# Optimization experiments

Hardware: AMD Instinct MI355X
Metric: run time of the kernel (lower is better)

## Reference

```python
import jax, jax.numpy as jnp
import numpy as np

N, T, K, V, E = 64, 256, 64, 32000, 100


def setup_inputs() -> dict:
    key = jax.random.key(0)
    ks = jax.random.split(key, 7)
    x = jax.random.randint(ks[0], (N, T), 0, V)
    emb_weight = jax.random.normal(ks[1], (V, E), dtype=jnp.float32)
    # trans: Linear(E, K*K, bias=False), weight uniform(-1,1)
    W_trans = jax.random.uniform(ks[2], (K * K, E), minval=-1.0, maxval=1.0, dtype=jnp.float32)
    # start: Linear(1, K)
    start_w = jax.random.normal(ks[3], (K, 1), dtype=jnp.float32) * 0.1
    start_b = jax.random.normal(ks[4], (K,), dtype=jnp.float32) * 0.1
    # emb_cluster: Embedding(K, K)
    emb_cluster_w = jax.random.normal(ks[5], (K, K), dtype=jnp.float32)
    # vocab: Linear(K, V, bias=False), weight uniform(-1,1)
    vocab_w = jax.random.uniform(ks[6], (V, K), minval=-1.0, maxval=1.0, dtype=jnp.float32)
    return {"x": x, "emb_weight": emb_weight, "W_trans": W_trans,
            "start_w": start_w, "start_b": start_b,
            "emb_cluster_w": emb_cluster_w, "vocab_w": vocab_w}


def reference(x, emb_weight, W_trans, start_w, start_b, emb_cluster_w, vocab_w):
    n, t = x.shape
    k = emb_cluster_w.shape[0]
    # word embeddings used to condition transitions at steps 0..T-2
    xe = emb_weight[x[:, :-1]]                                   # [N,T-1,E]
    # transition log-probs: log_softmax over destination state
    tran = jax.nn.log_softmax(
        jnp.einsum('nte,ce->ntc', xe, W_trans).reshape(n, t - 1, k, k), axis=-1)
    # emission log-probs per cluster: E[k, v]
    Elog = jax.nn.log_softmax(emb_cluster_w @ vocab_w.T, axis=-1)  # [K,V]
    emit = Elog.T[x[:, 1:]]                                       # [N,T-1,K]
    # initial alpha: log_softmax(start(ones)) expanded over batch
    alpha0 = jax.nn.log_softmax(start_w[:, 0] + start_b)           # [K]
    alpha0 = jnp.broadcast_to(alpha0[None, :], (n, k))
    tran_t = jnp.moveaxis(tran, 1, 0)   # [T-1,N,K,K]
    emit_t = jnp.moveaxis(emit, 1, 0)   # [T-1,N,K]

    def step(alpha, te):
        tr, em = te
        # logsumexp over previous state j: alpha[n,j] + tr[n,j,k]
        a = jax.scipy.special.logsumexp(alpha[:, :, None] + tr, axis=1) + em
        return a, None

    alpha, _ = jax.lax.scan(step, alpha0, (tran_t, emit_t))
    return -jnp.mean(jax.scipy.special.logsumexp(alpha, axis=1))
```

## Files before the change

kernel.cpp:

```cpp
#include <hip/hip_runtime.h>
#include <hip/hip_bf16.h>
#include <stdint.h>

#define NT 16320
#define NTPAD 16384
#define KDIM 128
#define NCOLS 4096
#define NSEQ 64
#define TSTEPS 255
#define VOCAB 32000
#define EDIM 100
#define CHUNKS 17
#define CLEN 15

typedef __attribute__((ext_vector_type(8))) short s8v;
typedef __attribute__((ext_vector_type(4))) float f4v;

__device__ __forceinline__ float bflo(uint32_t u) { return __uint_as_float(u << 16); }
__device__ __forceinline__ float bfhi(uint32_t u) { return __uint_as_float(u & 0xffff0000u); }

__device__ __forceinline__ void load_lds16(const void* g, void* l) {
    __builtin_amdgcn_global_load_lds(
        (const __attribute__((address_space(1))) void*)(uintptr_t)g,
        (__attribute__((address_space(3))) void*)(uintptr_t)l,
        16, 0, 0);
}

__global__ __launch_bounds__(256) void prep_dk(const int* __restrict__ x,
                                               const float* __restrict__ emb,
                                               const float* __restrict__ Wt,
                                               const float* __restrict__ ec,
                                               const float* __restrict__ vw,
                                               __hip_bfloat16* __restrict__ A,
                                               __hip_bfloat16* __restrict__ B,
                                               float* __restrict__ partials) {
    int bid = blockIdx.x;
    int tid = threadIdx.x;
    if (bid < 1280) {
        int rloc = tid >> 4, q = tid & 15;
        int b = bid * 16 + rloc;
        int c0 = q * 8;
        float vals[8] = {0.f, 0.f, 0.f, 0.f, 0.f, 0.f, 0.f, 0.f};
        __hip_bfloat16* dst;
        if (b < NTPAD) {
            if (b < NT) {
                int n = b / TSTEPS;
                int t = b - n * TSTEPS;
                int tok = x[n * 256 + t];
                const float* er = emb + (size_t)tok * EDIM;
#pragma unroll
                for (int i = 0; i < 8; ++i) { int e = c0 + i; if (e < EDIM) vals[i] = er[e]; }
            }
            dst = A + (size_t)b * KDIM + c0;
        } else {
            int cc = b - NTPAD;
            const float* wr = Wt + (size_t)cc * EDIM;
#pragma unroll
            for (int i = 0; i < 8; ++i) { int e = c0 + i; if (e < EDIM) vals[i] = wr[e]; }
            dst = B + (size_t)cc * KDIM + c0;
        }
        union { __hip_bfloat16 h[8]; uint4 u; } pk;
#pragma unroll
        for (int i = 0; i < 8; ++i) pk.h[i] = __float2bfloat16(vals[i]);
        *(uint4*)dst = pk.u;
    } else {
        int db = bid - 1280;
        int wave = tid >> 6, lane = tid & 63;
        float er[64];
        {
            const float4* ecv = (const float4*)(ec + (size_t)lane * 64);
#pragma unroll
            for (int i = 0; i < 16; ++i) {
                float4 v = ecv[i];
                er[4 * i] = v.x; er[4 * i + 1] = v.y; er[4 * i + 2] = v.z; er[4 * i + 3] = v.w;
            }
        }
        int v0 = db * 125;
        float m = -1e30f, s = 0.f;
        for (int v = v0 + wave; v < v0 + 125; v += 4) {
            int vu = __builtin_amdgcn_readfirstlane(v);
            const float* row = vw + (size_t)vu * 64;
            float acc = 0.f;
#pragma unroll
            for (int e = 0; e < 64; ++e) acc += er[e] * row[e];
            float nm = fmaxf(m, acc);
            s = s * __expf(m - nm) + __expf(acc - nm);
            m = nm;
        }
        __shared__ float pm[4][64], ps[4][64];
        pm[wave][lane] = m; ps[wave][lane] = s;
        __syncthreads();
        if (tid < 64) {
            float M = pm[0][tid], Ssum = ps[0][tid];
#pragma unroll
            for (int w = 1; w < 4; ++w) {
                float m2 = pm[w][tid], s2 = ps[w][tid];
                float nm = fmaxf(M, m2);
                Ssum = Ssum * __expf(M - nm) + s2 * __expf(m2 - nm);
                M = nm;
            }
            partials[(db * 64 + tid) * 2]     = M;
            partials[(db * 64 + tid) * 2 + 1] = Ssum;
        }
    }
}

__global__ __launch_bounds__(256) void emit_kern(const int* __restrict__ x,
                                                 const float* __restrict__ ec,
                                                 const float* __restrict__ vw,
                                                 const float* __restrict__ partials,
                                                 __hip_bfloat16* __restrict__ emB) {
    __shared__ float pm[4][64], ps[4][64], sD[64];
    int tid = threadIdx.x;
    int wave = tid >> 6, lane = tid & 63;

    {
        float M = -1e30f, S = 0.f;
        for (int b = wave; b < 256; b += 4) {
            float m2 = partials[(b * 64 + lane) * 2];
            float s2 = partials[(b * 64 + lane) * 2 + 1];
            float nm = fmaxf(M, m2);
            S = S * __expf(M - nm) + s2 * __expf(m2 - nm);
            M = nm;
        }
        pm[wave][lane] = M; ps[wave][lane] = S;
    }

    float er[64];
    {
        const float4* ecv = (const float4*)(ec + (size_t)lane * 64);
#pragma unroll
        for (int i = 0; i < 16; ++i) {
            float4 v = ecv[i];
            er[4 * i] = v.x; er[4 * i + 1] = v.y; er[4 * i + 2] = v.z; er[4 * i + 3] = v.w;
        }
    }
    __syncthreads();
    if (tid < 64) {
        float M = pm[0][tid], S = ps[0][tid];
#pragma unroll
        for (int w = 1; w < 4; ++w) {
            float m2 = pm[w][tid], s2 = ps[w][tid];
            float nm = fmaxf(M, m2);
            S = S * __expf(M - nm) + s2 * __expf(m2 - nm);
            M = nm;
        }
        sD[tid] = M + __logf(S);
    }
    __syncthreads();

    float dj = sD[lane];
    int j = lane;
    int pos = ((j >> 2) & 3) * 16 + ((j >> 4) & 3) * 4 + (j & 3);
    int nt0 = blockIdx.x * 32 + wave * 8;
#pragma unroll
    for (int s = 0; s < 8; ++s) {
        int nt = nt0 + s;
        int n = nt / TSTEPS;
        int t = nt - n * TSTEPS;
        int tok = x[n * 256 + t + 1];
        tok = __builtin_amdgcn_readfirstlane(tok);
        const float* row = vw + (size_t)tok * 64;
        float acc = 0.f;
#pragma unroll
        for (int e = 0; e < 64; ++e) acc += er[e] * row[e];
        emB[(size_t)nt * 64 + pos] = __float2bfloat16(__expf(acc - dj));
    }
}

__global__ __launch_bounds__(256) void gemm_kern(const __hip_bfloat16* __restrict__ A,
                                                 const __hip_bfloat16* __restrict__ B,
                                                 const __hip_bfloat16* __restrict__ emB,
                                                 __hip_bfloat16* __restrict__ Eg) {
    int mblk = blockIdx.x;
    int nblk = blockIdx.y;
    int tid = threadIdx.x, wave = tid >> 6, lane = tid & 63;

    __shared__ __align__(16) char smem[65536];
    char* sA = smem;
    char* sB = smem + 32768;

    {
        int r0 = wave * 32;
        int l16 = lane & 15;
        int rsub = lane >> 4;
#pragma unroll
        for (int g = 0; g < 8; ++g) {
            int r = r0 + g * 4 + rsub;
            int chunk = l16 ^ (r & 7);
            const char* gp = (const char*)(A + (size_t)(mblk * 128 + r) * KDIM) + chunk * 16;
            load_lds16(gp, sA + (r0 + g * 4) * 256);
        }
#pragma unroll
        for (int g = 0; g < 8; ++g) {
            int c = r0 + g * 4 + rsub;
            int chunk = l16 ^ (c & 7);
            const char* gp = (const char*)(B + (size_t)(nblk * 128 + c) * KDIM) + chunk * 16;
            load_lds16(gp, sB + (r0 + g * 4) * 256);
        }
    }
    __syncthreads();

    int wc = (wave >> 1) * 64, wm = (wave & 1) * 64;
    int l15 = lane & 15, g4 = lane >> 4;
    f4v acc[4][4] = {};
#pragma unroll
    for (int k32 = 0; k32 < 4; ++k32) {
        s8v af[4], bf[4];
#pragma unroll
        for (int jt = 0; jt < 4; ++jt) {
            int r = wc + jt * 16 + l15;
            int chunk = (k32 * 4 + g4) ^ (r & 7);
            af[jt] = *(const s8v*)(sB + r * 256 + chunk * 16);
        }
#pragma unroll
        for (int mt = 0; mt < 4; ++mt) {
            int r = wm + mt * 16 + l15;
            int chunk = (k32 * 4 + g4) ^ (r & 7);
            bf[mt] = *(const s8v*)(sA + r * 256 + chunk * 16);
        }
#pragma unroll
        for (int jt = 0; jt < 4; ++jt)
#pragma unroll
            for (int mt = 0; mt < 4; ++mt)
                acc[jt][mt] = __builtin_amdgcn_mfma_f32_16x16x32_bf16(af[jt], bf[mt], acc[jt][mt], 0, 0, 0);
    }
    __syncthreads();

    char* sW = smem;
    const char* emb8 = (const char*)emB;
#pragma unroll
    for (int mt = 0; mt < 4; ++mt) {
        int mrow = wm + mt * 16 + l15;
        int mglob = mblk * 128 + mrow;
        float v[16];
#pragma unroll
        for (int jt = 0; jt < 4; ++jt)
#pragma unroll
            for (int rr = 0; rr < 4; ++rr) v[jt * 4 + rr] = acc[jt][mt][rr];
        float mx = v[0];
#pragma unroll
        for (int k = 1; k < 16; ++k) mx = fmaxf(mx, v[k]);
        mx = fmaxf(mx, __shfl_xor(mx, 16, 64));
        mx = fmaxf(mx, __shfl_xor(mx, 32, 64));
        float ex[16], sg = 0.f;
#pragma unroll
        for (int k = 0; k < 16; ++k) { ex[k] = __expf(v[k] - mx); sg += ex[k]; }
        sg += __shfl_xor(sg, 16, 64);
        sg += __shfl_xor(sg, 32, 64);
        float inv = 1.0f / sg;
        uint4 e0 = *(const uint4*)(emb8 + (size_t)mglob * 128 + g4 * 32);
        uint4 e1 = *(const uint4*)(emb8 + (size_t)mglob * 128 + g4 * 32 + 16);
        float em[16];
        {
            const uint32_t* w0 = (const uint32_t*)&e0;
            const uint32_t* w1 = (const uint32_t*)&e1;
#pragma unroll
            for (int i = 0; i < 4; ++i) {
                em[2 * i] = bflo(w0[i]);     em[2 * i + 1] = bfhi(w0[i]);
                em[8 + 2 * i] = bflo(w1[i]); em[8 + 2 * i + 1] = bfhi(w1[i]);
            }
        }
#pragma unroll
        for (int jt = 0; jt < 4; ++jt) {
            union { __hip_bfloat16 h[4]; uint2 u; } pk;
#pragma unroll
            for (int rr = 0; rr < 4; ++rr)
                pk.h[rr] = __float2bfloat16(ex[jt * 4 + rr] * inv * em[jt * 4 + rr]);
            *(uint2*)(sW + mrow * 272 + (wc + jt * 16 + g4 * 4) * 2) = pk.u;
        }
    }
    __syncthreads();

    {
        int rloc = tid >> 3;
        int q = tid & 7;
#pragma unroll
        for (int rp = 0; rp < 4; ++rp) {
            int row = rp * 32 + rloc;
            char* dst = (char*)Eg + (size_t)(mblk * 128 + row) * 8192 + nblk * 256;
            const char* src = sW + row * 272;
            *(uint4*)(dst + q * 16)       = *(const uint4*)(src + q * 16);
            *(uint4*)(dst + 128 + q * 16) = *(const uint4*)(src + 128 + q * 16);
        }
    }
}

__global__ __launch_bounds__(64) void chunk_kern(const __hip_bfloat16* __restrict__ Eg,
                                                 __hip_bfloat16* __restrict__ Gout,
                                                 float* __restrict__ Rout,
                                                 float* __restrict__ out) {
    int lane = threadIdx.x;
    if (blockIdx.x == 0 && lane == 0) *out = 0.f;
    int l15 = lane & 15, g4 = lane >> 4;
    int id = blockIdx.x;
    int n = (id * 3856) >> 16;
    int c = id - n * 17;
    int base_m = n * TSTEPS + c * CLEN;

    __shared__ __align__(16) char sGT[64 * 144];

    {
        uint4 z = {0, 0, 0, 0};
#pragma unroll
        for (int i = 0; i < 8; ++i) *(uint4*)(sGT + lane * 144 + i * 16) = z;
        *(uint16_t*)(sGT + lane * 144 + lane * 2) = 0x3F80;
    }

    const char* Ebase = (const char*)Eg;
    uint4 pf[4][2];
    {
        const char* tp = Ebase + (size_t)(base_m + 14) * 8192;
#pragma unroll
        for (int at = 0; at < 4; ++at)
#pragma unroll
            for (int kk = 0; kk < 2; ++kk)
                pf[at][kk] = *(const uint4*)(tp + (at * 16 + l15) * 128 + kk * 64 + g4 * 16);
    }

    float rlog[4] = {0.f, 0.f, 0.f, 0.f};

    for (int tl = 14; tl >= 0; --tl) {
        uint4 af[4][2];
#pragma unroll
        for (int at = 0; at < 4; ++at) { af[at][0] = pf[at][0]; af[at][1] = pf[at][1]; }
        if (tl > 0) {
            const char* tp = Ebase + (size_t)(base_m + tl - 1) * 8192;
#pragma unroll
            for (int at = 0; at < 4; ++at)
#pragma unroll
                for (int kk = 0; kk < 2; ++kk)
                    pf[at][kk] = *(const uint4*)(tp + (at * 16 + l15) * 128 + kk * 64 + g4 * 16);
        }

        f4v acc[4][4] = {};
#pragma unroll
        for (int kk = 0; kk < 2; ++kk) {
#pragma unroll
            for (int ct = 0; ct < 4; ++ct) {
                s8v b = *(const s8v*)(sGT + (ct * 16 + l15) * 144 + kk * 64 + g4 * 16);
#pragma unroll
                for (int at = 0; at < 4; ++at)
                    acc[at][ct] = __builtin_amdgcn_mfma_f32_16x16x32_bf16(
                        *(const s8v*)&af[at][kk], b, acc[at][ct], 0, 0, 0);
            }
        }

        if (tl % 3 == 0) {
#pragma unroll
            for (int ct = 0; ct < 4; ++ct) {
                float mx = acc[0][ct][0];
#pragma unroll
                for (int at = 0; at < 4; ++at)
#pragma unroll
                    for (int rr = 0; rr < 4; ++rr) mx = fmaxf(mx, acc[at][ct][rr]);
                mx = fmaxf(mx, __shfl_xor(mx, 16, 64));
                mx = fmaxf(mx, __shfl_xor(mx, 32, 64));
                mx = fmaxf(mx, 1e-38f);
                rlog[ct] += __logf(mx);
                float inv = 1.0f / mx;
                int col = ct * 16 + l15;
#pragma unroll
                for (int at = 0; at < 4; ++at) {
                    union { __hip_bfloat16 h[4]; uint2 u; } pk;
#pragma unroll
                    for (int rr = 0; rr < 4; ++rr)
                        pk.h[rr] = __float2bfloat16(acc[at][ct][rr] * inv);
                    *(uint2*)(sGT + col * 144 + at * 32 + g4 * 8) = pk.u;
                }
            }
        } else {
#pragma unroll
            for (int ct = 0; ct < 4; ++ct) {
                int col = ct * 16 + l15;
#pragma unroll
                for (int at = 0; at < 4; ++at) {
                    union { __hip_bfloat16 h[4]; uint2 u; } pk;
#pragma unroll
                    for (int rr = 0; rr < 4; ++rr)
                        pk.h[rr] = __float2bfloat16(acc[at][ct][rr]);
                    *(uint2*)(sGT + col * 144 + at * 32 + g4 * 8) = pk.u;
                }
            }
        }
    }

    {
        char* go = (char*)(Gout + (size_t)id * 4096 + lane * 64);
#pragma unroll
        for (int i = 0; i < 8; ++i)
            *(uint4*)(go + i * 16) = *(const uint4*)(sGT + lane * 144 + i * 16);
    }
    if (g4 == 0)
#pragma unroll
        for (int ct = 0; ct < 4; ++ct)
            Rout[(size_t)id * 64 + ct * 16 + l15] = rlog[ct];
}

__global__ __launch_bounds__(64) void combine_kern(const __hip_bfloat16* __restrict__ G,
                                                   const float* __restrict__ R,
                                                   const float* __restrict__ sw,
                                                   const float* __restrict__ sb,
                                                   float* __restrict__ out) {
    int n = blockIdx.x;
    int lane = threadIdx.x;
    __shared__ __align__(16) float sV[64];

    float alpha;
    {
        float v = sw[lane] + sb[lane];
        float m = v;
#pragma unroll
        for (int off = 1; off < 64; off <<= 1) m = fmaxf(m, __shfl_xor(m, off, 64));
        float s = __expf(v - m);
#pragma unroll
        for (int off = 1; off < 64; off <<= 1) s += __shfl_xor(s, off, 64);
        alpha = v - (m + __logf(s));
    }

    const char* Gb = (const char*)(G + (size_t)n * CHUNKS * 4096) + lane * 128;
    const float* Rb = R + (size_t)n * CHUNKS * 64 + lane;

    uint4 pf[8];
#pragma unroll
    for (int i = 0; i < 8; ++i) pf[i] = *(const uint4*)(Gb + i * 16);
    float rpf = Rb[0];

    for (int c = 0; c < CHUNKS; ++c) {
        uint4 cur[8];
#pragma unroll
        for (int i = 0; i < 8; ++i) cur[i] = pf[i];
        float rc = rpf;
        if (c + 1 < CHUNKS) {
            const char* gn = Gb + (size_t)(c + 1) * 8192;
#pragma unroll
            for (int i = 0; i < 8; ++i) pf[i] = *(const uint4*)(gn + i * 16);
            rpf = Rb[(c + 1) * 64];
        }

        float m = alpha;
#pragma unroll
        for (int off = 1; off < 64; off <<= 1) m = fmaxf(m, __shfl_xor(m, off, 64));
        sV[lane] = __expf(alpha - m);
        float acc = 0.f;
        const float4* sv4 = (const float4*)sV;
#pragma unroll
        for (int i = 0; i < 8; ++i) {
            const uint32_t* gw = (const uint32_t*)&cur[i];
            float4 va = sv4[2 * i], vb = sv4[2 * i + 1];
            acc += va.x * bflo(gw[0]) + va.y * bfhi(gw[0]);
            acc += va.z * bflo(gw[1]) + va.w * bfhi(gw[1]);
            acc += vb.x * bflo(gw[2]) + vb.y * bfhi(gw[2]);
            acc += vb.z * bflo(gw[3]) + vb.w * bfhi(gw[3]);
        }
        alpha = m + __logf(fmaxf(acc, 1e-38f)) + rc;
    }

    {
        float m = alpha;
#pragma unroll
        for (int off = 1; off < 64; off <<= 1) m = fmaxf(m, __shfl_xor(m, off, 64));
        float s = __expf(alpha - m);
#pragma unroll
        for (int off = 1; off < 64; off <<= 1) s += __shfl_xor(s, off, 64);
        if (lane == 0) atomicAdd(out, -(m + __logf(s)) * (1.0f / 64.0f));
    }
}

extern "C" void kernel_launch(void* const* d_in, const int* in_sizes, int n_in,
                              void* d_out, int out_size, void* d_ws, size_t ws_size,
                              hipStream_t stream) {
    const int*   x   = (const int*)d_in[0];
    const float* emb = (const float*)d_in[1];
    const float* Wt  = (const float*)d_in[2];
    const float* sw  = (const float*)d_in[3];
    const float* sb  = (const float*)d_in[4];
    const float* ec  = (const float*)d_in[5];
    const float* vw  = (const float*)d_in[6];
    float* out = (float*)d_out;
    char* ws = (char*)d_ws;

    __hip_bfloat16* Eg  = (__hip_bfloat16*)ws;
    __hip_bfloat16* A   = (__hip_bfloat16*)(ws + 134217728ull);
    __hip_bfloat16* B   = (__hip_bfloat16*)(ws + 138412032ull);
    __hip_bfloat16* emB = (__hip_bfloat16*)(ws + 139460608ull);
    float* partials     = (float*)(ws + 141557760ull);
    __hip_bfloat16* Gc  = (__hip_bfloat16*)(ws + 141688832ull);
    float* Rc           = (float*)(ws + 150601728ull);

    prep_dk<<<1536, 256, 0, stream>>>(x, emb, Wt, ec, vw, A, B, partials);
    emit_kern<<<510, 256, 0, stream>>>(x, ec, vw, partials, emB);
    gemm_kern<<<dim3(NTPAD / 128, NCOLS / 128), 256, 0, stream>>>(A, B, emB, Eg);
    chunk_kern<<<NSEQ * CHUNKS, 64, 0, stream>>>(Eg, Gc, Rc, out);
    combine_kern<<<NSEQ, 64, 0, stream>>>(Gc, Rc, sw, sb, out);
}
```

Measured before the change: 212.6 us.

## Halve gemm N-tile to 64 columns, cut LDS, and drop softmax max-subtraction

```diff
diff --git a/kernel.cpp b/kernel.cpp
--- a/kernel.cpp
+++ b/kernel.cpp
@@ -168,22 +168,22 @@
     }
 }
 
-__global__ __launch_bounds__(256) void gemm_kern(const __hip_bfloat16* __restrict__ A,
-                                                 const __hip_bfloat16* __restrict__ B,
-                                                 const __hip_bfloat16* __restrict__ emB,
-                                                 __hip_bfloat16* __restrict__ Eg) {
+__global__ __launch_bounds__(256, 3) void gemm_kern(const __hip_bfloat16* __restrict__ A,
+                                                    const __hip_bfloat16* __restrict__ B,
+                                                    const __hip_bfloat16* __restrict__ emB,
+                                                    __hip_bfloat16* __restrict__ Eg) {
     int mblk = blockIdx.x;
     int nblk = blockIdx.y;
     int tid = threadIdx.x, wave = tid >> 6, lane = tid & 63;
 
-    __shared__ __align__(16) char smem[65536];
+    __shared__ __align__(16) char smem[49152];
     char* sA = smem;
     char* sB = smem + 32768;
 
     {
-        int r0 = wave * 32;
         int l16 = lane & 15;
         int rsub = lane >> 4;
+        int r0 = wave * 32;
 #pragma unroll
         for (int g = 0; g < 8; ++g) {
             int r = r0 + g * 4 + rsub;
@@ -191,30 +191,31 @@
             const char* gp = (const char*)(A + (size_t)(mblk * 128 + r) * KDIM) + chunk * 16;
             load_lds16(gp, sA + (r0 + g * 4) * 256);
         }
-#pragma unroll
-        for (int g = 0; g < 8; ++g) {
-            int c = r0 + g * 4 + rsub;
-            int chunk = l16 ^ (c & 7);
-            const char* gp = (const char*)(B + (size_t)(nblk * 128 + c) * KDIM) + chunk * 16;
-            load_lds16(gp, sB + (r0 + g * 4) * 256);
+        int rb0 = wave * 16;
+#pragma unroll
+        for (int g = 0; g < 4; ++g) {
+            int r = rb0 + g * 4 + rsub;
+            int chunk = l16 ^ (r & 7);
+            const char* gp = (const char*)(B + (size_t)(nblk * 64 + r) * KDIM) + chunk * 16;
+            load_lds16(gp, sB + (rb0 + g * 4) * 256);
         }
     }
     __syncthreads();
 
-    int wc = (wave >> 1) * 64, wm = (wave & 1) * 64;
+    int wm = wave * 32;
     int l15 = lane & 15, g4 = lane >> 4;
-    f4v acc[4][4] = {};
+    f4v acc[4][2] = {};
 #pragma unroll
     for (int k32 = 0; k32 < 4; ++k32) {
-        s8v af[4], bf[4];
+        s8v af[4], bf[2];
 #pragma unroll
         for (int jt = 0; jt < 4; ++jt) {
-            int r = wc + jt * 16 + l15;
+            int r = jt * 16 + l15;
             int chunk = (k32 * 4 + g4) ^ (r & 7);
             af[jt] = *(const s8v*)(sB + r * 256 + chunk * 16);
         }
 #pragma unroll
-        for (int mt = 0; mt < 4; ++mt) {
+        for (int mt = 0; mt < 2; ++mt) {
             int r = wm + mt * 16 + l15;
             int chunk = (k32 * 4 + g4) ^ (r & 7);
             bf[mt] = *(const s8v*)(sA + r * 256 + chunk * 16);
@@ -222,7 +223,7 @@
 #pragma unroll
         for (int jt = 0; jt < 4; ++jt)
 #pragma unroll
-            for (int mt = 0; mt < 4; ++mt)
+            for (int mt = 0; mt < 2; ++mt)
                 acc[jt][mt] = __builtin_amdgcn_mfma_f32_16x16x32_bf16(af[jt], bf[mt], acc[jt][mt], 0, 0, 0);
     }
     __syncthreads();
@@ -230,22 +231,17 @@
     char* sW = smem;
     const char* emb8 = (const char*)emB;
 #pragma unroll
-    for (int mt = 0; mt < 4; ++mt) {
+    for (int mt = 0; mt < 2; ++mt) {
         int mrow = wm + mt * 16 + l15;
         int mglob = mblk * 128 + mrow;
-        float v[16];
+        float ex[16], sg = 0.f;
 #pragma unroll
         for (int jt = 0; jt < 4; ++jt)
 #pragma unroll
-            for (int rr = 0; rr < 4; ++rr) v[jt * 4 + rr] = acc[jt][mt][rr];
-        float mx = v[0];
-#pragma unroll
-        for (int k = 1; k < 16; ++k) mx = fmaxf(mx, v[k]);
-        mx = fmaxf(mx, __shfl_xor(mx, 16, 64));
-        mx = fmaxf(mx, __shfl_xor(mx, 32, 64));
-        float ex[16], sg = 0.f;
-#pragma unroll
-        for (int k = 0; k < 16; ++k) { ex[k] = __expf(v[k] - mx); sg += ex[k]; }
+            for (int rr = 0; rr < 4; ++rr) {
+                float e = __expf(acc[jt][mt][rr]);
+                ex[jt * 4 + rr] = e; sg += e;
+            }
         sg += __shfl_xor(sg, 16, 64);
         sg += __shfl_xor(sg, 32, 64);
         float inv = 1.0f / sg;
@@ -267,7 +263,7 @@
 #pragma unroll
             for (int rr = 0; rr < 4; ++rr)
                 pk.h[rr] = __float2bfloat16(ex[jt * 4 + rr] * inv * em[jt * 4 + rr]);
-            *(uint2*)(sW + mrow * 272 + (wc + jt * 16 + g4 * 4) * 2) = pk.u;
+            *(uint2*)(sW + mrow * 144 + (jt * 16 + g4 * 4) * 2) = pk.u;
         }
     }
     __syncthreads();
@@ -278,10 +274,8 @@
 #pragma unroll
         for (int rp = 0; rp < 4; ++rp) {
             int row = rp * 32 + rloc;
-            char* dst = (char*)Eg + (size_t)(mblk * 128 + row) * 8192 + nblk * 256;
-            const char* src = sW + row * 272;
-            *(uint4*)(dst + q * 16)       = *(const uint4*)(src + q * 16);
-            *(uint4*)(dst + 128 + q * 16) = *(const uint4*)(src + 128 + q * 16);
+            char* dst = (char*)Eg + (size_t)(mblk * 128 + row) * 8192 + nblk * 128;
+            *(uint4*)(dst + q * 16) = *(const uint4*)(sW + row * 144 + q * 16);
         }
     }
 }
@@ -490,7 +484,7 @@
 
     prep_dk<<<1536, 256, 0, stream>>>(x, emb, Wt, ec, vw, A, B, partials);
     emit_kern<<<510, 256, 0, stream>>>(x, ec, vw, partials, emB);
-    gemm_kern<<<dim3(NTPAD / 128, NCOLS / 128), 256, 0, stream>>>(A, B, emB, Eg);
+    gemm_kern<<<dim3(128, 64), 256, 0, stream>>>(A, B, emB, Eg);
     chunk_kern<<<NSEQ * CHUNKS, 64, 0, stream>>>(Eg, Gc, Rc, out);
     combine_kern<<<NSEQ, 64, 0, stream>>>(Gc, Rc, sw, sb, out);
 }
```

After: 209.0 us, median of 2. Within noise of the previous version (-1.7%).
